# Performance work log

Hardware: AMD Instinct MI355X
Metric: run time of the kernel (lower is better)

## Reference

```python
import jax, jax.numpy as jnp
import numpy as np

N = 4096      # total nodes
NPG = 64      # nodes per graph
B = 64        # graphs in batch
D = 256       # d_features
P1 = 32       # pooling size level 1
P2 = 8        # pooling size level 2
E = 65536     # edges
DLIN = 512
DOUT = 256


def setup_inputs() -> dict:
    key = jax.random.key(0)
    ks = jax.random.split(key, 16)
    x = jax.random.normal(ks[0], (N, D), jnp.float32)
    # edges within each graph's contiguous node segment
    base = (jnp.arange(E) % B) * NPG
    src = base + jax.random.randint(ks[1], (E,), 0, NPG)
    dst = base + jax.random.randint(ks[2], (E,), 0, NPG)
    edge_index = jnp.stack([src, dst]).astype(jnp.int32)
    batch = (jnp.arange(N) // NPG).astype(jnp.int32)

    def w(k, i, o):
        return (jax.random.normal(k, (i, o), jnp.float32) / np.sqrt(i)).astype(jnp.float32)

    return {
        "x": x, "edge_index": edge_index, "batch": batch,
        "pool0_W1": w(ks[3], D, D), "pool0_W2": w(ks[4], D, P1),
        "emb0_W1": w(ks[5], D, D), "emb0_W2": w(ks[6], D, D),
        "pool1_W1": w(ks[7], D, D), "pool1_W2": w(ks[8], D, P2),
        "emb1_W1": w(ks[9], D, D), "emb1_W2": w(ks[10], D, D),
        "lin1_W": w(ks[11], D, DLIN), "lin1_b": jnp.zeros((DLIN,), jnp.float32),
        "lin2_W": w(ks[12], DLIN, DOUT), "lin2_b": jnp.zeros((DOUT,), jnp.float32),
    }


def _gnn(X, A, W1, W2):
    # GATEncoder stand-in: two adjacency propagation + linear steps
    H = jax.nn.relu((A @ X + X) @ W1)
    return (A @ H + H) @ W2


def _block_diag(blocks):
    # blocks: (b, s, s) -> dense block-diagonal (b*s, b*s)
    b, s, _ = blocks.shape
    out = jnp.zeros((b, s, b, s), blocks.dtype)
    out = out.at[jnp.arange(b), :, jnp.arange(b), :].set(blocks)
    return out.reshape(b * s, b * s)


def _extract_blocks(A, size, bsz):
    return A.reshape(bsz, size, bsz, size)[jnp.arange(bsz), :, jnp.arange(bsz), :]


def reference(x, edge_index, batch, pool0_W1, pool0_W2, emb0_W1, emb0_W2,
              pool1_W1, pool1_W2, emb1_W1, emb1_W2, lin1_W, lin1_b, lin2_W, lin2_b):
    # dense adjacency scatter-build
    A = jnp.zeros((N, N), x.dtype).at[edge_index[0], edge_index[1]].set(1.0)

    # --- diffpool level 1 (ankward_diffpool; equal-size segments -> batched bmm) ---
    S = jax.nn.softmax(_gnn(x, A, pool0_W1, pool0_W2), axis=-1)   # (N, P1)
    Z = _gnn(x, A, emb0_W1, emb0_W2)                              # (N, D)
    Sb = S.reshape(B, NPG, P1)
    Zb = Z.reshape(B, NPG, D)
    Ab = _extract_blocks(A, NPG, B)                               # (B, NPG, NPG)
    X = jnp.einsum('bns,bnd->bsd', Sb, Zb).reshape(B * P1, D)
    A = _block_diag(jnp.einsum('bns,bnm,bmt->bst', Sb, Ab, Sb))   # (B*P1, B*P1)

    # --- diffpool level 2 (batch_diffpool) ---
    S2 = jax.nn.softmax(_gnn(X, A, pool1_W1, pool1_W2).reshape(B, P1, P2), axis=-1)
    Z2 = _gnn(X, A, emb1_W1, emb1_W2).reshape(B, P1, D)
    Ab2 = _extract_blocks(A, P1, B)                               # (B, P1, P1)
    X = jnp.einsum('bns,bnd->bsd', S2, Z2).reshape(B * P2, D)
    _ = _block_diag(jnp.einsum('bns,bnm,bmt->bst', S2, Ab2, S2))  # built as in original (unused downstream)

    # global mean pool over the regular coarse batch, then final MLP (dropout=eval -> identity)
    Xg = X.reshape(B, P2, D).mean(axis=1)                         # (B, D)
    return jax.nn.relu(Xg @ lin1_W + lin1_b) @ lin2_W + lin2_b    # (B, DOUT)
```

## Files before the change

kernel.cpp:

```cpp
#include <hip/hip_runtime.h>

typedef __attribute__((ext_vector_type(8))) short bfx8;
typedef __attribute__((ext_vector_type(4))) short bfx4;
typedef __attribute__((ext_vector_type(4))) float fx4;
typedef __attribute__((ext_vector_type(4))) int   ix4;

#define OA   0
#define OB0  8192
#define OB1  40960
#define OB2  73728
#define OB3  106496
#define OSP  139264
#define OST  147456
#define OX2  OB1
#define OAS  (OB1+16384)
#define OA2  (OB1+20480)
#define OV   (OB1+22528)
#define OW   (OB1+22656)
#define OU   (OB1+23680)
#define OT1  (OB1+24704)
#define LDS_TOTAL 151552

__device__ __forceinline__ short f2bf(float f){
    union{float f;unsigned u;}v; v.f=f;
    unsigned r = v.u + 0x7FFFu + ((v.u>>16)&1u);
    return (short)(r>>16);
}
__device__ __forceinline__ float bf2f(short s){
    union{unsigned u;float f;}v; v.u = ((unsigned)(unsigned short)s)<<16; return v.f;
}

__device__ __forceinline__ int so16(int r,int c,int pitch){ return ((r*pitch+c)*2) ^ ((r&7)<<4); }
__device__ __forceinline__ int so32(int r,int c,int pitch){ return ((r*pitch+c)*4) ^ ((r&7)<<4); }
__device__ __forceinline__ int mpoff(int r,int c){
    int base = (c&128)? OB2 : OB0;
    return base + so32(r, c&127, 128);
}

__device__ __forceinline__ bfx8 ldfrag(const char* sm,int boff,int r0,int k0,int pitch,int lane){
    int r = r0 + (lane&15);
    int c = k0 + ((lane>>4)<<3);
    return *(const bfx8*)(sm + boff + so16(r,c,pitch));
}

__device__ __forceinline__ void gemm_ll(const char* sm,int aoff,int ap,int boff,int bp,
                                        int NT,int K,int lane,int w,fx4* acc,int TPW,bool add){
    for(int i=0;i<TPW;i++){
        int t=w*TPW+i; int mt=t/NT, nt=t%NT;
        fx4 c; if(add) c=acc[i]; else c=fx4{0.f,0.f,0.f,0.f};
        for(int ks=0; ks<K; ks+=32){
            bfx8 a = ldfrag(sm,aoff,mt<<4,ks,ap,lane);
            bfx8 b = ldfrag(sm,boff,nt<<4,ks,bp,lane);
            c = __builtin_amdgcn_mfma_f32_16x16x32_bf16(a,b,c,0,0,0);
        }
        acc[i]=c;
    }
}
__device__ __forceinline__ void gemm_lg(const char* sm,int aoff,int ap,const bfx8* pk,
                                        int NT,int K,int lane,int w,fx4* acc,int TPW,bool add){
    int KT = K>>5;
    for(int i=0;i<TPW;i++){
        int t=w*TPW+i; int mt=t/NT, nt=t%NT;
        fx4 c; if(add) c=acc[i]; else c=fx4{0.f,0.f,0.f,0.f};
        for(int ks=0; ks<KT; ks++){
            bfx8 a = ldfrag(sm,aoff,mt<<4,ks<<5,ap,lane);
            bfx8 b = pk[(nt*KT+ks)*64 + lane];
            c = __builtin_amdgcn_mfma_f32_16x16x32_bf16(a,b,c,0,0,0);
        }
        acc[i]=c;
    }
}

__device__ __forceinline__ void st_norm(char* sm,int boff,int pitch,int NT,int lane,int w,int TPW,
                                        const fx4* acc,bool relu){
    for(int i=0;i<TPW;i++){
        int t=w*TPW+i; int mt=t/NT, nt=t%NT;
        int col=(nt<<4)+(lane&15), rb=(mt<<4)+((lane>>4)<<2);
        for(int q=0;q<4;q++){
            float v=acc[i][q]; if(relu) v=fmaxf(v,0.f);
            *(short*)(sm+boff+so16(rb+q,col,pitch)) = f2bf(v);
        }
    }
}
__device__ __forceinline__ void st_norm_hilo(char* sm,int bhi,int blo,int pitch,int NT,int lane,int w,
                                             int TPW,const fx4* acc,bool relu){
    for(int i=0;i<TPW;i++){
        int t=w*TPW+i; int mt=t/NT, nt=t%NT;
        int col=(nt<<4)+(lane&15), rb=(mt<<4)+((lane>>4)<<2);
        for(int q=0;q<4;q++){
            float v=acc[i][q]; if(relu) v=fmaxf(v,0.f);
            short hi=f2bf(v);
            *(short*)(sm+bhi+so16(rb+q,col,pitch)) = hi;
            *(short*)(sm+blo+so16(rb+q,col,pitch)) = f2bf(v - bf2f(hi));
        }
    }
}
__device__ __forceinline__ void st_tr(char* sm,int boff,int pitch,int NT,int lane,int w,int TPW,
                                      const fx4* acc,bool relu){
    for(int i=0;i<TPW;i++){
        int t=w*TPW+i; int mt=t/NT, nt=t%NT;
        int rn=(nt<<4)+(lane&15), cb=(mt<<4)+((lane>>4)<<2);
        bfx4 p;
        for(int q=0;q<4;q++){ float v=acc[i][q]; if(relu) v=fmaxf(v,0.f); p[q]=f2bf(v); }
        *(bfx4*)(sm+boff+so16(rn,cb,pitch)) = p;
    }
}
__device__ __forceinline__ void st_tr_hilo(char* sm,int bhi,int blo,int pitch,int NT,int lane,int w,
                                           int TPW,const fx4* acc,bool relu){
    for(int i=0;i<TPW;i++){
        int t=w*TPW+i; int mt=t/NT, nt=t%NT;
        int rn=(nt<<4)+(lane&15), cb=(mt<<4)+((lane>>4)<<2);
        bfx4 ph, pl;
        for(int q=0;q<4;q++){
            float v=acc[i][q]; if(relu) v=fmaxf(v,0.f);
            short hi=f2bf(v); ph[q]=hi; pl[q]=f2bf(v - bf2f(hi));
        }
        *(bfx4*)(sm+bhi+so16(rn,cb,pitch)) = ph;
        *(bfx4*)(sm+blo+so16(rn,cb,pitch)) = pl;
    }
}
__device__ __forceinline__ void st_mp(char* sm,int NT,int lane,int w,int TPW,const fx4* acc){
    for(int i=0;i<TPW;i++){
        int t=w*TPW+i; int mt=t/NT, nt=t%NT;
        int col=(nt<<4)+(lane&15), rb=(mt<<4)+((lane>>4)<<2);
        for(int q=0;q<4;q++) *(float*)(sm+mpoff(rb+q,col)) = acc[i][q];
    }
}

__global__ __launch_bounds__(256) void prepack_k(const float* __restrict__ Wp1,const float* __restrict__ We1,
                                                 const float* __restrict__ We2,const float* __restrict__ We21,
                                                 short* __restrict__ outp){
    int g = blockIdx.x; int seg = g>>5;
    int t = ((g&31)<<8) + threadIdx.x;
    int lane = t&63, tile = t>>6, kt = tile&7, nt = tile>>3;
    const float* W = (seg<2)? Wp1 : (seg==2)? We1 : (seg==3)? We2 : We21;
    int kb  = (kt<<5) + ((lane>>4)<<3);
    int col = (nt<<4) + (lane&15);
    bfx8 o;
#pragma unroll
    for(int j=0;j<8;j++){
        float v = W[(kb+j)*256 + col];
        short hi = f2bf(v);
        o[j] = (seg==1)? f2bf(v - bf2f(hi)) : hi;
    }
    ((bfx8*)outp)[seg*8192 + t] = o;
}

__global__ __launch_bounds__(512) void mega_k(const float* __restrict__ x, const int* __restrict__ ei,
        const float* __restrict__ Wp2,  const float* __restrict__ We22,
        const float* __restrict__ l1W,  const float* __restrict__ l1b,
        const float* __restrict__ l2W,  const float* __restrict__ l2b,
        const short* __restrict__ pks,  float* __restrict__ out){
    extern __shared__ char sm[];
    const int tid = threadIdx.x, lane = tid&63, w = tid>>6, b = blockIdx.x;
    const bfx8* pkWp1hi = (const bfx8*)pks;
    const bfx8* pkWp1lo = pkWp1hi + 8192;
    const bfx8* pkWe1   = pkWp1hi + 16384;
    const bfx8* pkWe2   = pkWp1hi + 24576;
    const bfx8* pkWe21  = pkWp1hi + 32768;
    fx4 acc[8];

    *(ix4*)(sm + OA + tid*16) = ix4{0,0,0,0};
    for(int ch=0; ch<32; ch++){
        int i = tid + (ch<<9); int r = i>>8, c = i&255;
        *(short*)(sm + OB0 + so16(c, r, 64)) = f2bf(x[(((b<<6)+r)<<8) + c]);
    }
    __syncthreads();
    for(int q=0;q<2;q++){
        int e = b + (((tid<<1)+q)<<6);
        int s = ei[e]&63, d = ei[e+65536]&63;
        *(short*)(sm + OA + so16(s, d, 64)) = (short)0x3F80;
    }
    __syncthreads();
    if(tid<64){
        int off = OA + so16(tid, tid, 64);
        *(short*)(sm+off) = f2bf(bf2f(*(short*)(sm+off)) + 1.0f);
    }
    __syncthreads();

    gemm_ll(sm, OA,64, OB0,64, 16,64, lane,w, acc,8,false);
    st_norm_hilo(sm, OB1, OB2, 256, 16, lane,w,8, acc, false);
    __syncthreads();

    gemm_lg(sm, OB1,256, pkWe1, 16,256, lane,w, acc,8,false);
    st_tr(sm, OB3, 64, 16, lane,w,8, acc, true);
    gemm_lg(sm, OB1,256, pkWp1hi, 16,256, lane,w, acc,8,false);
    gemm_lg(sm, OB1,256, pkWp1lo, 16,256, lane,w, acc,8,true);
    gemm_lg(sm, OB2,256, pkWp1hi, 16,256, lane,w, acc,8,true);
    __syncthreads();
    st_tr_hilo(sm, OB0, OB2, 64, 16, lane,w,8, acc, true);
    __syncthreads();

    gemm_ll(sm, OA,64, OB0,64, 16,64, lane,w, acc,8,false);
    gemm_ll(sm, OA,64, OB2,64, 16,64, lane,w, acc,8,true);
    __syncthreads();
    st_mp(sm, 16, lane,w,8, acc);
    __syncthreads();

    {
        int r = tid>>3, sg = tid&7;
        float a0=0.f,a1=0.f,a2=0.f,a3=0.f;
        for(int c=0;c<256;c++){
            float m = *(const float*)(sm + mpoff(r,c));
            fx4 wv = *(const fx4*)(Wp2 + (c<<5) + (sg<<2));
            a0 += m*wv[0]; a1 += m*wv[1]; a2 += m*wv[2]; a3 += m*wv[3];
        }
        *(float*)(sm+OSP+so32(r,(sg<<2)+0,32))=a0;
        *(float*)(sm+OSP+so32(r,(sg<<2)+1,32))=a1;
        *(float*)(sm+OSP+so32(r,(sg<<2)+2,32))=a2;
        *(float*)(sm+OSP+so32(r,(sg<<2)+3,32))=a3;
    }
    __syncthreads();
    {
        int r = tid>>3, j = tid&7;
        float v0=*(const float*)(sm+OSP+so32(r,(j<<2)+0,32));
        float v1=*(const float*)(sm+OSP+so32(r,(j<<2)+1,32));
        float v2=*(const float*)(sm+OSP+so32(r,(j<<2)+2,32));
        float v3=*(const float*)(sm+OSP+so32(r,(j<<2)+3,32));
        float mx = fmaxf(fmaxf(v0,v1),fmaxf(v2,v3));
        for(int o=1;o<8;o<<=1) mx = fmaxf(mx, __shfl_xor(mx,o,64));
        float e0=__expf(v0-mx), e1=__expf(v1-mx), e2=__expf(v2-mx), e3=__expf(v3-mx);
        float s = e0+e1+e2+e3;
        for(int o=1;o<8;o<<=1) s += __shfl_xor(s,o,64);
        float inv = 1.f/s;
        *(short*)(sm+OST+so16((j<<2)+0,r,64)) = f2bf(e0*inv);
        *(short*)(sm+OST+so16((j<<2)+1,r,64)) = f2bf(e1*inv);
        *(short*)(sm+OST+so16((j<<2)+2,r,64)) = f2bf(e2*inv);
        *(short*)(sm+OST+so16((j<<2)+3,r,64)) = f2bf(e3*inv);
    }
    __syncthreads();

    gemm_ll(sm, OA,64, OB3,64, 16,64, lane,w, acc,8,false);
    st_norm(sm, OB1, 256, 16, lane,w,8, acc, false);
    __syncthreads();
    gemm_lg(sm, OB1,256, pkWe2, 16,256, lane,w, acc,8,false);
    st_tr(sm, OB2, 64, 16, lane,w,8, acc, false);
    __syncthreads();
    gemm_ll(sm, OST,64, OB2,64, 16,64, lane,w, acc,4,false);
    st_tr(sm, OX2, 32, 16, lane,w,4, acc, false);
    __syncthreads();
    {
        gemm_ll(sm, OA,64, OST,64, 2,64, lane,w, acc,1,false);
        int mt = w>>1, nt = w&1;
        int tcol = (nt<<4)+(lane&15), cb = (mt<<4)+((lane>>4)<<2);
        bfx4 p;
        for(int q=0;q<4;q++){
            float v = acc[0][q] - bf2f(*(const short*)(sm+OST+so16(tcol,cb+q,64)));
            p[q]=f2bf(v);
        }
        *(bfx4*)(sm+OAS+so16(tcol,cb,64)) = p;
    }
    __syncthreads();
    if(w<4){
        gemm_ll(sm, OST,64, OAS,64, 2,64, lane,w, acc,1,false);
        int mt=w>>1, nt=w&1;
        int col=(nt<<4)+(lane&15), rb=(mt<<4)+((lane>>4)<<2);
        for(int q=0;q<4;q++){
            float v = acc[0][q] + ((rb+q)==col ? 1.f : 0.f);
            *(short*)(sm+OA2+so16(rb+q,col,32)) = f2bf(v);
        }
    }
    __syncthreads();
    if(tid<32){
        float s=0.f;
        for(int r=0;r<32;r++) s += bf2f(*(const short*)(sm+OA2+so16(r,tid,32)));
        *(float*)(sm+OV+(tid<<2)) = s;
    }
    __syncthreads();
    gemm_ll(sm, OA2,32, OX2,32, 16,32, lane,w, acc,4,false);
    st_norm(sm, OB3, 256, 16, lane,w,4, acc, false);
    __syncthreads();
    gemm_lg(sm, OB3,256, pkWe21, 16,256, lane,w, acc,4,false);
    st_norm(sm, OB0, 256, 16, lane,w,4, acc, true);
    __syncthreads();
    if(tid<256){
        float a=0.f;
        for(int n=0;n<32;n++)
            a += *(const float*)(sm+OV+(n<<2)) * bf2f(*(const short*)(sm+OB0+so16(n,tid,256)));
        *(float*)(sm+OW+(tid<<2)) = a;
    }
    __syncthreads();
    if(tid<256){
        float a=0.f;
        for(int k=0;k<256;k++) a += *(const float*)(sm+OW+(k<<2)) * We22[(k<<8)+tid];
        *(float*)(sm+OU+(tid<<2)) = 0.125f*a;
    }
    __syncthreads();
    {
        float a = l1b[tid];
        for(int k=0;k<256;k++) a += *(const float*)(sm+OU+(k<<2)) * l1W[(k<<9)+tid];
        *(float*)(sm+OT1+(tid<<2)) = fmaxf(a,0.f);
    }
    __syncthreads();
    if(tid<256){
        float a = l2b[tid];
        for(int k=0;k<512;k++) a += *(const float*)(sm+OT1+(k<<2)) * l2W[(k<<8)+tid];
        out[(b<<8)+tid] = a;
    }
}

extern "C" void kernel_launch(void* const* d_in, const int* in_sizes, int n_in,
                              void* d_out, int out_size, void* d_ws, size_t ws_size,
                              hipStream_t stream) {
    const float* x    = (const float*)d_in[0];
    const int*   ei   = (const int*)d_in[1];
    const float* p0W1 = (const float*)d_in[3];
    const float* p0W2 = (const float*)d_in[4];
    const float* e0W1 = (const float*)d_in[5];
    const float* e0W2 = (const float*)d_in[6];
    const float* e1W1 = (const float*)d_in[9];
    const float* e1W2 = (const float*)d_in[10];
    const float* l1W  = (const float*)d_in[11];
    const float* l1b  = (const float*)d_in[12];
    const float* l2W  = (const float*)d_in[13];
    const float* l2b  = (const float*)d_in[14];
    float* out = (float*)d_out;
    short* pks = (short*)d_ws;

    hipFuncSetAttribute((const void*)mega_k, hipFuncAttributeMaxDynamicSharedMemorySize, LDS_TOTAL);
    prepack_k<<<160, 256, 0, stream>>>(p0W1, e0W1, e0W2, e1W1, pks);
    mega_k<<<64, 512, LDS_TOTAL, stream>>>(x, ei, p0W2, e1W2, l1W, l1b, l2W, l2b, pks, out);
}
```

Baseline: 201.9 us.

## Double block threads to 1024 and template MFMA GEMM helpers for full unrolling

Raises the per-block thread count from 512 to 1024 so each wave handles half as many MFMA tiles (TPW 8→4), which increases the wave count available to hide latency in the single 64-block launch. GEMM and store helpers become templates with compile-time tile counts and fully unrolled loops, and the x load is vectorized to float4. Scalar phases are guarded to keep their original thread ranges. The cost is higher register pressure under a 1024-thread launch bound, plus more threads idling during the serial stages.

```diff
diff --git a/kernel.cpp b/kernel.cpp
--- a/kernel.cpp
+++ b/kernel.cpp
@@ -43,50 +43,61 @@
     return *(const bfx8*)(sm + boff + so16(r,c,pitch));
 }
 
-__device__ __forceinline__ void gemm_ll(const char* sm,int aoff,int ap,int boff,int bp,
-                                        int NT,int K,int lane,int w,fx4* acc,int TPW,bool add){
-    for(int i=0;i<TPW;i++){
-        int t=w*TPW+i; int mt=t/NT, nt=t%NT;
-        fx4 c; if(add) c=acc[i]; else c=fx4{0.f,0.f,0.f,0.f};
-        for(int ks=0; ks<K; ks+=32){
-            bfx8 a = ldfrag(sm,aoff,mt<<4,ks,ap,lane);
-            bfx8 b = ldfrag(sm,boff,nt<<4,ks,bp,lane);
+template<int NTL,int KS,int TPW,bool ADD>
+__device__ __forceinline__ void gemm_ll_t(const char* sm,int aoff,int ap,int boff,int bp,
+                                          int lane,int w,fx4* acc){
+#pragma unroll
+    for(int i=0;i<TPW;i++){
+        int t=w*TPW+i, mt=t>>NTL, nt=t&((1<<NTL)-1);
+        fx4 c = ADD? acc[i] : fx4{0.f,0.f,0.f,0.f};
+#pragma unroll
+        for(int ks=0;ks<KS;ks++){
+            bfx8 a = ldfrag(sm,aoff,mt<<4,ks<<5,ap,lane);
+            bfx8 b = ldfrag(sm,boff,nt<<4,ks<<5,bp,lane);
             c = __builtin_amdgcn_mfma_f32_16x16x32_bf16(a,b,c,0,0,0);
         }
         acc[i]=c;
     }
 }
-__device__ __forceinline__ void gemm_lg(const char* sm,int aoff,int ap,const bfx8* pk,
-                                        int NT,int K,int lane,int w,fx4* acc,int TPW,bool add){
-    int KT = K>>5;
-    for(int i=0;i<TPW;i++){
-        int t=w*TPW+i; int mt=t/NT, nt=t%NT;
-        fx4 c; if(add) c=acc[i]; else c=fx4{0.f,0.f,0.f,0.f};
-        for(int ks=0; ks<KT; ks++){
+template<int NTL,int KS,int TPW,bool ADD>
+__device__ __forceinline__ void gemm_lg_t(const char* sm,int aoff,int ap,const bfx8* pk,
+                                          int lane,int w,fx4* acc){
+#pragma unroll
+    for(int i=0;i<TPW;i++){
+        int t=w*TPW+i, mt=t>>NTL, nt=t&((1<<NTL)-1);
+        fx4 c = ADD? acc[i] : fx4{0.f,0.f,0.f,0.f};
+#pragma unroll
+        for(int ks=0;ks<KS;ks++){
             bfx8 a = ldfrag(sm,aoff,mt<<4,ks<<5,ap,lane);
-            bfx8 b = pk[(nt*KT+ks)*64 + lane];
+            bfx8 b = pk[(nt*KS+ks)*64 + lane];
             c = __builtin_amdgcn_mfma_f32_16x16x32_bf16(a,b,c,0,0,0);
         }
         acc[i]=c;
     }
 }
 
-__device__ __forceinline__ void st_norm(char* sm,int boff,int pitch,int NT,int lane,int w,int TPW,
+template<int NTL,int TPW>
+__device__ __forceinline__ void st_norm(char* sm,int boff,int pitch,int lane,int w,
                                         const fx4* acc,bool relu){
-    for(int i=0;i<TPW;i++){
-        int t=w*TPW+i; int mt=t/NT, nt=t%NT;
+#pragma unroll
+    for(int i=0;i<TPW;i++){
+        int t=w*TPW+i, mt=t>>NTL, nt=t&((1<<NTL)-1);
         int col=(nt<<4)+(lane&15), rb=(mt<<4)+((lane>>4)<<2);
+#pragma unroll
         for(int q=0;q<4;q++){
             float v=acc[i][q]; if(relu) v=fmaxf(v,0.f);
             *(short*)(sm+boff+so16(rb+q,col,pitch)) = f2bf(v);
         }
     }
 }
-__device__ __forceinline__ void st_norm_hilo(char* sm,int bhi,int blo,int pitch,int NT,int lane,int w,
-                                             int TPW,const fx4* acc,bool relu){
-    for(int i=0;i<TPW;i++){
-        int t=w*TPW+i; int mt=t/NT, nt=t%NT;
+template<int NTL,int TPW>
+__device__ __forceinline__ void st_norm_hilo(char* sm,int bhi,int blo,int pitch,int lane,int w,
+                                             const fx4* acc,bool relu){
+#pragma unroll
+    for(int i=0;i<TPW;i++){
+        int t=w*TPW+i, mt=t>>NTL, nt=t&((1<<NTL)-1);
         int col=(nt<<4)+(lane&15), rb=(mt<<4)+((lane>>4)<<2);
+#pragma unroll
         for(int q=0;q<4;q++){
             float v=acc[i][q]; if(relu) v=fmaxf(v,0.f);
             short hi=f2bf(v);
@@ -95,22 +106,28 @@
         }
     }
 }
-__device__ __forceinline__ void st_tr(char* sm,int boff,int pitch,int NT,int lane,int w,int TPW,
+template<int NTL,int TPW>
+__device__ __forceinline__ void st_tr(char* sm,int boff,int pitch,int lane,int w,
                                       const fx4* acc,bool relu){
-    for(int i=0;i<TPW;i++){
-        int t=w*TPW+i; int mt=t/NT, nt=t%NT;
+#pragma unroll
+    for(int i=0;i<TPW;i++){
+        int t=w*TPW+i, mt=t>>NTL, nt=t&((1<<NTL)-1);
         int rn=(nt<<4)+(lane&15), cb=(mt<<4)+((lane>>4)<<2);
         bfx4 p;
+#pragma unroll
         for(int q=0;q<4;q++){ float v=acc[i][q]; if(relu) v=fmaxf(v,0.f); p[q]=f2bf(v); }
         *(bfx4*)(sm+boff+so16(rn,cb,pitch)) = p;
     }
 }
-__device__ __forceinline__ void st_tr_hilo(char* sm,int bhi,int blo,int pitch,int NT,int lane,int w,
-                                           int TPW,const fx4* acc,bool relu){
-    for(int i=0;i<TPW;i++){
-        int t=w*TPW+i; int mt=t/NT, nt=t%NT;
+template<int NTL,int TPW>
+__device__ __forceinline__ void st_tr_hilo(char* sm,int bhi,int blo,int pitch,int lane,int w,
+                                           const fx4* acc,bool relu){
+#pragma unroll
+    for(int i=0;i<TPW;i++){
+        int t=w*TPW+i, mt=t>>NTL, nt=t&((1<<NTL)-1);
         int rn=(nt<<4)+(lane&15), cb=(mt<<4)+((lane>>4)<<2);
         bfx4 ph, pl;
+#pragma unroll
         for(int q=0;q<4;q++){
             float v=acc[i][q]; if(relu) v=fmaxf(v,0.f);
             short hi=f2bf(v); ph[q]=hi; pl[q]=f2bf(v - bf2f(hi));
@@ -119,10 +136,13 @@
         *(bfx4*)(sm+blo+so16(rn,cb,pitch)) = pl;
     }
 }
-__device__ __forceinline__ void st_mp(char* sm,int NT,int lane,int w,int TPW,const fx4* acc){
-    for(int i=0;i<TPW;i++){
-        int t=w*TPW+i; int mt=t/NT, nt=t%NT;
+template<int TPW>
+__device__ __forceinline__ void st_mp(char* sm,int lane,int w,const fx4* acc){
+#pragma unroll
+    for(int i=0;i<TPW;i++){
+        int t=w*TPW+i, mt=t>>4, nt=t&15;
         int col=(nt<<4)+(lane&15), rb=(mt<<4)+((lane>>4)<<2);
+#pragma unroll
         for(int q=0;q<4;q++) *(float*)(sm+mpoff(rb+q,col)) = acc[i][q];
     }
 }
@@ -146,7 +166,7 @@
     ((bfx8*)outp)[seg*8192 + t] = o;
 }
 
-__global__ __launch_bounds__(512) void mega_k(const float* __restrict__ x, const int* __restrict__ ei,
+__global__ __launch_bounds__(1024) void mega_k(const float* __restrict__ x, const int* __restrict__ ei,
         const float* __restrict__ Wp2,  const float* __restrict__ We22,
         const float* __restrict__ l1W,  const float* __restrict__ l1b,
         const float* __restrict__ l2W,  const float* __restrict__ l2b,
@@ -158,16 +178,21 @@
     const bfx8* pkWe1   = pkWp1hi + 16384;
     const bfx8* pkWe2   = pkWp1hi + 24576;
     const bfx8* pkWe21  = pkWp1hi + 32768;
-    fx4 acc[8];
-
-    *(ix4*)(sm + OA + tid*16) = ix4{0,0,0,0};
-    for(int ch=0; ch<32; ch++){
-        int i = tid + (ch<<9); int r = i>>8, c = i&255;
-        *(short*)(sm + OB0 + so16(c, r, 64)) = f2bf(x[(((b<<6)+r)<<8) + c]);
-    }
-    __syncthreads();
-    for(int q=0;q<2;q++){
-        int e = b + (((tid<<1)+q)<<6);
+    fx4 acc[4];
+
+    if(tid<512) *(ix4*)(sm + OA + tid*16) = ix4{0,0,0,0};
+#pragma unroll
+    for(int ch=0; ch<4; ch++){
+        int i2 = tid + (ch<<10);
+        int r = i2>>6, c0 = (i2&63)<<2;
+        fx4 v = *(const fx4*)(x + (size_t)(((b<<6)+r)<<8) + c0);
+#pragma unroll
+        for(int j=0;j<4;j++)
+            *(short*)(sm + OB0 + so16(c0+j, r, 64)) = f2bf(v[j]);
+    }
+    __syncthreads();
+    {
+        int e = b + (tid<<6);
         int s = ei[e]&63, d = ei[e+65536]&63;
         *(short*)(sm + OA + so16(s, d, 64)) = (short)0x3F80;
     }
@@ -178,26 +203,26 @@
     }
     __syncthreads();
 
-    gemm_ll(sm, OA,64, OB0,64, 16,64, lane,w, acc,8,false);
-    st_norm_hilo(sm, OB1, OB2, 256, 16, lane,w,8, acc, false);
-    __syncthreads();
-
-    gemm_lg(sm, OB1,256, pkWe1, 16,256, lane,w, acc,8,false);
-    st_tr(sm, OB3, 64, 16, lane,w,8, acc, true);
-    gemm_lg(sm, OB1,256, pkWp1hi, 16,256, lane,w, acc,8,false);
-    gemm_lg(sm, OB1,256, pkWp1lo, 16,256, lane,w, acc,8,true);
-    gemm_lg(sm, OB2,256, pkWp1hi, 16,256, lane,w, acc,8,true);
-    __syncthreads();
-    st_tr_hilo(sm, OB0, OB2, 64, 16, lane,w,8, acc, true);
-    __syncthreads();
-
-    gemm_ll(sm, OA,64, OB0,64, 16,64, lane,w, acc,8,false);
-    gemm_ll(sm, OA,64, OB2,64, 16,64, lane,w, acc,8,true);
-    __syncthreads();
-    st_mp(sm, 16, lane,w,8, acc);
-    __syncthreads();
-
-    {
+    gemm_ll_t<4,2,4,false>(sm, OA,64, OB0,64, lane,w, acc);
+    st_norm_hilo<4,4>(sm, OB1, OB2, 256, lane,w, acc, false);
+    __syncthreads();
+
+    gemm_lg_t<4,8,4,false>(sm, OB1,256, pkWe1, lane,w, acc);
+    st_tr<4,4>(sm, OB3, 64, lane,w, acc, true);
+    gemm_lg_t<4,8,4,false>(sm, OB1,256, pkWp1hi, lane,w, acc);
+    gemm_lg_t<4,8,4,true >(sm, OB1,256, pkWp1lo, lane,w, acc);
+    gemm_lg_t<4,8,4,true >(sm, OB2,256, pkWp1hi, lane,w, acc);
+    __syncthreads();
+    st_tr_hilo<4,4>(sm, OB0, OB2, 64, lane,w, acc, true);
+    __syncthreads();
+
+    gemm_ll_t<4,2,4,false>(sm, OA,64, OB0,64, lane,w, acc);
+    gemm_ll_t<4,2,4,true >(sm, OA,64, OB2,64, lane,w, acc);
+    __syncthreads();
+    st_mp<4>(sm, lane,w, acc);
+    __syncthreads();
+
+    if(tid<512){
         int r = tid>>3, sg = tid&7;
         float a0=0.f,a1=0.f,a2=0.f,a3=0.f;
         for(int c=0;c<256;c++){
@@ -211,16 +236,18 @@
         *(float*)(sm+OSP+so32(r,(sg<<2)+3,32))=a3;
     }
     __syncthreads();
-    {
+    if(tid<512){
         int r = tid>>3, j = tid&7;
         float v0=*(const float*)(sm+OSP+so32(r,(j<<2)+0,32));
         float v1=*(const float*)(sm+OSP+so32(r,(j<<2)+1,32));
         float v2=*(const float*)(sm+OSP+so32(r,(j<<2)+2,32));
         float v3=*(const float*)(sm+OSP+so32(r,(j<<2)+3,32));
         float mx = fmaxf(fmaxf(v0,v1),fmaxf(v2,v3));
+#pragma unroll
         for(int o=1;o<8;o<<=1) mx = fmaxf(mx, __shfl_xor(mx,o,64));
         float e0=__expf(v0-mx), e1=__expf(v1-mx), e2=__expf(v2-mx), e3=__expf(v3-mx);
         float s = e0+e1+e2+e3;
+#pragma unroll
         for(int o=1;o<8;o<<=1) s += __shfl_xor(s,o,64);
         float inv = 1.f/s;
         *(short*)(sm+OST+so16((j<<2)+0,r,64)) = f2bf(e0*inv);
@@ -230,20 +257,21 @@
     }
     __syncthreads();
 
-    gemm_ll(sm, OA,64, OB3,64, 16,64, lane,w, acc,8,false);
-    st_norm(sm, OB1, 256, 16, lane,w,8, acc, false);
-    __syncthreads();
-    gemm_lg(sm, OB1,256, pkWe2, 16,256, lane,w, acc,8,false);
-    st_tr(sm, OB2, 64, 16, lane,w,8, acc, false);
-    __syncthreads();
-    gemm_ll(sm, OST,64, OB2,64, 16,64, lane,w, acc,4,false);
-    st_tr(sm, OX2, 32, 16, lane,w,4, acc, false);
-    __syncthreads();
-    {
-        gemm_ll(sm, OA,64, OST,64, 2,64, lane,w, acc,1,false);
+    gemm_ll_t<4,2,4,false>(sm, OA,64, OB3,64, lane,w, acc);
+    st_norm<4,4>(sm, OB1, 256, lane,w, acc, false);
+    __syncthreads();
+    gemm_lg_t<4,8,4,false>(sm, OB1,256, pkWe2, lane,w, acc);
+    st_tr<4,4>(sm, OB2, 64, lane,w, acc, false);
+    __syncthreads();
+    gemm_ll_t<4,2,2,false>(sm, OST,64, OB2,64, lane,w, acc);
+    st_tr<4,2>(sm, OX2, 32, lane,w, acc, false);
+    __syncthreads();
+    if(w<8){
+        gemm_ll_t<1,2,1,false>(sm, OA,64, OST,64, lane,w, acc);
         int mt = w>>1, nt = w&1;
         int tcol = (nt<<4)+(lane&15), cb = (mt<<4)+((lane>>4)<<2);
         bfx4 p;
+#pragma unroll
         for(int q=0;q<4;q++){
             float v = acc[0][q] - bf2f(*(const short*)(sm+OST+so16(tcol,cb+q,64)));
             p[q]=f2bf(v);
@@ -252,9 +280,10 @@
     }
     __syncthreads();
     if(w<4){
-        gemm_ll(sm, OST,64, OAS,64, 2,64, lane,w, acc,1,false);
+        gemm_ll_t<1,2,1,false>(sm, OST,64, OAS,64, lane,w, acc);
         int mt=w>>1, nt=w&1;
         int col=(nt<<4)+(lane&15), rb=(mt<<4)+((lane>>4)<<2);
+#pragma unroll
         for(int q=0;q<4;q++){
             float v = acc[0][q] + ((rb+q)==col ? 1.f : 0.f);
             *(short*)(sm+OA2+so16(rb+q,col,32)) = f2bf(v);
@@ -263,18 +292,20 @@
     __syncthreads();
     if(tid<32){
         float s=0.f;
+#pragma unroll
         for(int r=0;r<32;r++) s += bf2f(*(const short*)(sm+OA2+so16(r,tid,32)));
         *(float*)(sm+OV+(tid<<2)) = s;
     }
     __syncthreads();
-    gemm_ll(sm, OA2,32, OX2,32, 16,32, lane,w, acc,4,false);
-    st_norm(sm, OB3, 256, 16, lane,w,4, acc, false);
-    __syncthreads();
-    gemm_lg(sm, OB3,256, pkWe21, 16,256, lane,w, acc,4,false);
-    st_norm(sm, OB0, 256, 16, lane,w,4, acc, true);
+    gemm_ll_t<4,1,2,false>(sm, OA2,32, OX2,32, lane,w, acc);
+    st_norm<4,2>(sm, OB3, 256, lane,w, acc, false);
+    __syncthreads();
+    gemm_lg_t<4,8,2,false>(sm, OB3,256, pkWe21, lane,w, acc);
+    st_norm<4,2>(sm, OB0, 256, lane,w, acc, true);
     __syncthreads();
     if(tid<256){
         float a=0.f;
+#pragma unroll
         for(int n=0;n<32;n++)
             a += *(const float*)(sm+OV+(n<<2)) * bf2f(*(const short*)(sm+OB0+so16(n,tid,256)));
         *(float*)(sm+OW+(tid<<2)) = a;
@@ -286,7 +317,7 @@
         *(float*)(sm+OU+(tid<<2)) = 0.125f*a;
     }
     __syncthreads();
-    {
+    if(tid<512){
         float a = l1b[tid];
         for(int k=0;k<256;k++) a += *(const float*)(sm+OU+(k<<2)) * l1W[(k<<9)+tid];
         *(float*)(sm+OT1+(tid<<2)) = fmaxf(a,0.f);
@@ -319,5 +350,5 @@
 
     hipFuncSetAttribute((const void*)mega_k, hipFuncAttributeMaxDynamicSharedMemorySize, LDS_TOTAL);
     prepack_k<<<160, 256, 0, stream>>>(p0W1, e0W1, e0W2, e1W1, pks);
-    mega_k<<<64, 512, LDS_TOTAL, stream>>>(x, ei, p0W2, e1W2, l1W, l1b, l2W, l2b, pks, out);
-}
+    mega_k<<<64, 1024, LDS_TOTAL, stream>>>(x, ei, p0W2, e1W2, l1W, l1b, l2W, l2b, pks, out);
+}
```

Result: faster. 193.8 us (-4.0%).
